# Kernel tuning notes

Hardware: AMD Instinct MI355X
Metric: run time of the kernel (lower is better)

## Reference

```python
import jax, jax.numpy as jnp
import numpy as np

N = 50000
E = 800000
IN_C = 128
HID_C = 64
OUT_C = 64
HEADS = 4
NEG_SLOPE = 0.2


def setup_inputs() -> dict:
    key = jax.random.key(0)
    ks = jax.random.split(key, 12)
    x = jax.random.normal(ks[0], (N, IN_C), dtype=jnp.float32)
    edge_index = jax.random.randint(ks[1], (2, E), 0, N, dtype=jnp.int32)
    s = 0.1
    # layer 1 params (GATConv: shared lin for src/dst, att vectors per head, bias over H*C)
    W1 = jax.random.normal(ks[2], (IN_C, HEADS * HID_C), dtype=jnp.float32) * s
    att_src1 = jax.random.normal(ks[3], (HEADS, HID_C), dtype=jnp.float32) * s
    att_dst1 = jax.random.normal(ks[4], (HEADS, HID_C), dtype=jnp.float32) * s
    b1 = jnp.zeros((HEADS * HID_C,), dtype=jnp.float32)
    # layer 2 params
    W2 = jax.random.normal(ks[5], (HEADS * HID_C, HEADS * OUT_C), dtype=jnp.float32) * s
    att_src2 = jax.random.normal(ks[6], (HEADS, OUT_C), dtype=jnp.float32) * s
    att_dst2 = jax.random.normal(ks[7], (HEADS, OUT_C), dtype=jnp.float32) * s
    b2 = jnp.zeros((HEADS * OUT_C,), dtype=jnp.float32)
    return {"x": x, "edge_index": edge_index,
            "W1": W1, "att_src1": att_src1, "att_dst1": att_dst1, "b1": b1,
            "W2": W2, "att_src2": att_src2, "att_dst2": att_dst2, "b2": b2}


def _segment_softmax(e, dst, n):
    # e: [E, H], softmax over edges sharing the same dst node, per head
    m = jax.ops.segment_max(e, dst, num_segments=n)        # [N, H]
    ex = jnp.exp(e - m[dst])
    z = jax.ops.segment_sum(ex, dst, num_segments=n)       # [N, H]
    return ex / (z[dst] + 1e-16)


def _gat_layer(x, src, dst, W, att_src, att_dst, bias, heads, out_c):
    n = x.shape[0]
    h = (x @ W).reshape(n, heads, out_c)                   # [N, H, C]
    a_s = jnp.einsum('nhc,hc->nh', h, att_src)             # [N, H]
    a_d = jnp.einsum('nhc,hc->nh', h, att_dst)
    e = jax.nn.leaky_relu(a_s[src] + a_d[dst], NEG_SLOPE)  # [E, H]
    alpha = _segment_softmax(e, dst, n)                    # [E, H]
    msg = alpha[:, :, None] * h[src]                       # [E, H, C]
    out = jax.ops.segment_sum(msg, dst, num_segments=n)    # [N, H, C]
    return out.reshape(n, heads * out_c) + bias


def reference(x, edge_index, W1, att_src1, att_dst1, b1, W2, att_src2, att_dst2, b2):
    # PyG GATConv adds self-loops by default
    loops = jnp.arange(N, dtype=edge_index.dtype)
    src = jnp.concatenate([edge_index[0], loops])
    dst = jnp.concatenate([edge_index[1], loops])
    h = jax.nn.elu(_gat_layer(x, src, dst, W1, att_src1, att_dst1, b1, HEADS, HID_C))
    out = jax.nn.elu(_gat_layer(h, src, dst, W2, att_src2, att_dst2, b2, HEADS, OUT_C))
    return out  # [N, HEADS*OUT_C]
```

## Files before the change

kernel.cpp:

```cpp
#include <hip/hip_runtime.h>
#include <hip/hip_fp16.h>
#include <math.h>


#define LEAKY_SLOPE 0.2f

typedef __attribute__((ext_vector_type(8))) short short8v;
typedef __attribute__((ext_vector_type(8))) _Float16 half8v;
typedef __attribute__((ext_vector_type(4))) float float4v;


__global__ void prep_kernel(const float* __restrict__ W1, __half* __restrict__ Bt1,
                            const float* __restrict__ W2, __half* __restrict__ Bt2,
                            const float* __restrict__ x, __half* __restrict__ x_h,
                            const int* __restrict__ ei, int* __restrict__ cnt,
                            int E, int N, int xblocks) {
    int b = blockIdx.x;
    if (b < 128) {
        int idx = b * 256 + threadIdx.x;
        int k = idx >> 8, c = idx & 255;
        Bt1[c * 128 + k] = __float2half(W1[idx]);
    } else if (b < 384) {
        int idx = (b - 128) * 256 + threadIdx.x;
        int k = idx >> 8, c = idx & 255;
        Bt2[c * 256 + k] = __float2half(W2[idx]);
    } else if (b < 384 + xblocks) {
        int t = (b - 384) * 256 + threadIdx.x;
        if (t < N * 32) {
            float4 v = *(const float4*)&x[(size_t)t * 4];
            __half2 h01 = __floats2half2_rn(v.x, v.y);
            __half2 h23 = __floats2half2_rn(v.z, v.w);
            uint2 pk = {*(unsigned*)&h01, *(unsigned*)&h23};
            *(uint2*)&x_h[(size_t)t * 4] = pk;
        }
    } else {
        int e = (b - 384 - xblocks) * 256 + threadIdx.x;
        if (e < E + N) {
            int dst = (e < E) ? ei[E + e] : (e - E);
            atomicAdd(&cnt[dst], 1);
        }
    }
}


__global__ __launch_bounds__(1024) void scan_block(const int* __restrict__ cnt,
                                                   int* __restrict__ row_start,
                                                   int* __restrict__ partials,
                                                   int n) {
    __shared__ int wsum[16];
    int tid = threadIdx.x, lane = tid & 63, wid = tid >> 6;
    int gi = blockIdx.x * 1024 + tid;
    int v = (gi < n) ? ((cnt[gi] + 1) & ~1) : 0;
    int x = v;
#pragma unroll
    for (int off = 1; off < 64; off <<= 1) {
        int y = __shfl_up(x, off, 64);
        if (lane >= off) x += y;
    }
    if (lane == 63) wsum[wid] = x;
    __syncthreads();
    if (wid == 0 && lane < 16) {
        int w = wsum[lane];
#pragma unroll
        for (int off = 1; off < 16; off <<= 1) {
            int y = __shfl_up(w, off, 16);
            if (lane >= off) w += y;
        }
        wsum[lane] = w;
    }
    __syncthreads();
    int excl = x - v + ((wid > 0) ? wsum[wid - 1] : 0);
    if (gi < n) row_start[gi] = excl;
    if (tid == 1023) partials[blockIdx.x] = wsum[15];
}

__global__ __launch_bounds__(1024) void scan_add(int* __restrict__ row_start,
                                                 const int* __restrict__ partials,
                                                 int n, int nb) {
    __shared__ int spart[2];
    if (threadIdx.x < 64) {
        int lane = threadIdx.x;
        int v = (lane < nb) ? partials[lane] : 0;
        int x = v;
#pragma unroll
        for (int off = 1; off < 64; off <<= 1) {
            int y = __shfl_up(x, off, 64);
            if (lane >= off) x += y;
        }
        if (lane == (int)blockIdx.x) spart[0] = x - v;
        if (lane == nb - 1) spart[1] = x;
    }
    __syncthreads();
    int gi = blockIdx.x * 1024 + threadIdx.x;
    if (gi < n) row_start[gi] += spart[0];
    if (gi == 0) row_start[n] = spart[1];
}

__global__ void scatter_kernel(const int* __restrict__ ei,
                               const int* __restrict__ row_start,
                               int* __restrict__ fill,
                               int2* __restrict__ edge_sd, int E, int Etot) {
    int e = blockIdx.x * blockDim.x + threadIdx.x;
    if (e >= Etot) return;
    int src, dst;
    if (e < E) { src = ei[e]; dst = ei[E + e]; }
    else       { src = e - E; dst = e - E; }
    int pos = row_start[dst] + atomicAdd(&fill[dst], 1);
    edge_sd[pos] = make_int2(src, dst);
}

__device__ __forceinline__ uint4 make_rec(int src, int dst,
                                          const __half* __restrict__ a_s_h,
                                          const float* __restrict__ a_d) {
    if (src < 0) {
        uint4 z = {0u, 0u, 0u, 0u};
        return z;
    }
    uint2 as2 = *(const uint2*)&a_s_h[(size_t)src * 4];
    float4 ad4 = *(const float4*)&a_d[(size_t)dst * 4];
    float2 f01 = __half22float2(*(const __half2*)&as2.x);
    float2 f23 = __half22float2(*(const __half2*)&as2.y);
    float e0 = f01.x + ad4.x, e1 = f01.y + ad4.y;
    float e2 = f23.x + ad4.z, e3 = f23.y + ad4.w;
    e0 = (e0 > 0.f) ? e0 : LEAKY_SLOPE * e0;
    e1 = (e1 > 0.f) ? e1 : LEAKY_SLOPE * e1;
    e2 = (e2 > 0.f) ? e2 : LEAKY_SLOPE * e2;
    e3 = (e3 > 0.f) ? e3 : LEAKY_SLOPE * e3;
    __half2 w01 = __floats2half2_rn(__expf(e0), __expf(e1));
    __half2 w23 = __floats2half2_rn(__expf(e2), __expf(e3));
    uint4 r = {(unsigned)src, *(unsigned*)&w01, *(unsigned*)&w23, 0u};
    return r;
}

__global__ void fill_rec(const int4* __restrict__ edge_sd2,
                         const __half* __restrict__ a_s_h,
                         const float* __restrict__ a_d,
                         uint4* __restrict__ rec, int npairs) {
    int i = blockIdx.x * blockDim.x + threadIdx.x;
    if (i >= npairs) return;
    int4 sd = edge_sd2[i];
    uint4 r0 = make_rec(sd.x, sd.y, a_s_h, a_d);
    uint4 r1 = make_rec(sd.z, sd.w, a_s_h, a_d);
    rec[2 * i] = r0;
    rec[2 * i + 1] = r1;
}


template <int K>
__global__ __launch_bounds__(256) void gemm_mfma(
    const __half* __restrict__ Ah, const __half* __restrict__ Bt,
    __half* __restrict__ Ch,
    const float* __restrict__ att_src, const float* __restrict__ att_dst,
    __half* __restrict__ a_s_out, float* __restrict__ a_d_out, int M) {
    __shared__ short As[128][40];
    __shared__ short Bs[128][40];

    const int col0 = (blockIdx.x & 1) * 128;
    const int row0 = (blockIdx.x >> 1) * 128;
    const int tid = threadIdx.x;
    const int lane = tid & 63;
    const int wave = tid >> 6;
    const int wr = wave >> 1, wc = wave & 1;
    const int quad = lane >> 4, lc = lane & 15;

    float4v acc[4][4] = {};

    const short* Abits = (const short*)Ah;
    const short* Bbits = (const short*)Bt;

    const int sr = tid >> 2;
    const int ko = (tid & 3) * 8;
    const int ga0 = row0 + sr, ga1 = ga0 + 64;
    const size_t gb0 = (size_t)(col0 + sr) * K + ko;
    const size_t gb1 = (size_t)(col0 + sr + 64) * K + ko;

    short8v pa0, pa1, pb0, pb1;
#define LOADT(k0)                                                          \
    {                                                                      \
        pa0 = {}; pa1 = {};                                                \
        if (ga0 < M) pa0 = *(const short8v*)&Abits[(size_t)ga0 * K + (k0) + ko]; \
        if (ga1 < M) pa1 = *(const short8v*)&Abits[(size_t)ga1 * K + (k0) + ko]; \
        pb0 = *(const short8v*)&Bbits[gb0 + (k0)];                         \
        pb1 = *(const short8v*)&Bbits[gb1 + (k0)];                         \
    }

    LOADT(0);

#pragma unroll
    for (int k0 = 0; k0 < K; k0 += 32) {
        *(short8v*)&As[sr][ko] = pa0;
        *(short8v*)&As[sr + 64][ko] = pa1;
        *(short8v*)&Bs[sr][ko] = pb0;
        *(short8v*)&Bs[sr + 64][ko] = pb1;
        __syncthreads();

        if (k0 + 32 < K) LOADT(k0 + 32);

        half8v a[4], bv[4];
#pragma unroll
        for (int mt = 0; mt < 4; mt++) {
            int r = wr * 64 + mt * 16 + lc;
            a[mt] = *(const half8v*)&As[r][quad * 8];
        }
#pragma unroll
        for (int nt = 0; nt < 4; nt++) {
            int n = wc * 64 + nt * 16 + lc;
            bv[nt] = *(const half8v*)&Bs[n][quad * 8];
        }
#pragma unroll
        for (int mt = 0; mt < 4; mt++)
#pragma unroll
            for (int nt = 0; nt < 4; nt++)
                acc[mt][nt] = __builtin_amdgcn_mfma_f32_16x16x32_f16(
                    a[mt], bv[nt], acc[mt][nt], 0, 0, 0);
        __syncthreads();
    }
#undef LOADT

    const int head = (col0 >> 6) + wc;
    float as_c[4], ad_c[4];
#pragma unroll
    for (int nt = 0; nt < 4; nt++) {
        as_c[nt] = att_src[head * 64 + nt * 16 + lc];
        ad_c[nt] = att_dst[head * 64 + nt * 16 + lc];
    }

#pragma unroll
    for (int mt = 0; mt < 4; mt++) {
#pragma unroll
        for (int r = 0; r < 4; r++) {
            int gr = row0 + wr * 64 + mt * 16 + quad * 4 + r;
            float ps = 0.f, pd = 0.f;
#pragma unroll
            for (int nt = 0; nt < 4; nt++) {
                float c = acc[mt][nt][r];
                ps = fmaf(c, as_c[nt], ps);
                pd = fmaf(c, ad_c[nt], pd);
                if (gr < M)
                    Ch[(size_t)gr * 256 + col0 + wc * 64 + nt * 16 + lc] =
                        __float2half(c);
            }
#pragma unroll
            for (int off = 1; off < 16; off <<= 1) {
                ps += __shfl_xor(ps, off, 64);
                pd += __shfl_xor(pd, off, 64);
            }
            if (lc == 0 && gr < M) {
                a_s_out[gr * 4 + head] = __float2half(ps);
                a_d_out[gr * 4 + head] = pd;
            }
        }
    }
}


template <bool OUT_HALF>
__global__ __launch_bounds__(256) void gat_aggregate(
    const __half* __restrict__ hh, const uint4* __restrict__ rec,
    const int* __restrict__ row_start, const float* __restrict__ bias,
    void* __restrict__ outp, int n) {
    int node = (blockIdx.x * blockDim.x + threadIdx.x) >> 6;
    if (node >= n) return;
    int lane = threadIdx.x & 63;
    int half = lane >> 5, l32 = lane & 31;
    int head = l32 >> 3;
    unsigned wsh = (head & 1) << 4;

    int beg = row_start[node];
    int end = row_start[node + 1];

    float l = 0.f;
    float acc[8] = {};

    uint4 r0 = rec[beg + half];
    uint4 r1 = rec[beg + 2 + half];
    uint4 r2 = rec[beg + 4 + half];
    uint4 r3 = rec[beg + 6 + half];

#define GATH(rr) (*(const uint4*)&hh[(size_t)(rr).x * 256 + l32 * 8])
#define PROC(rr, vv)                                                      \
    {                                                                     \
        unsigned u = (head & 2) ? (rr).z : (rr).y;                        \
        unsigned short us = (unsigned short)(u >> wsh);                   \
        float w = __half2float(*(const __half*)&us);                      \
        l += w;                                                           \
        const __half2* hp = (const __half2*)&(vv);                        \
        float2 f0 = __half22float2(hp[0]);                                \
        float2 f1 = __half22float2(hp[1]);                                \
        float2 f2 = __half22float2(hp[2]);                                \
        float2 f3 = __half22float2(hp[3]);                                \
        acc[0] = fmaf(w, f0.x, acc[0]); acc[1] = fmaf(w, f0.y, acc[1]);   \
        acc[2] = fmaf(w, f1.x, acc[2]); acc[3] = fmaf(w, f1.y, acc[3]);   \
        acc[4] = fmaf(w, f2.x, acc[4]); acc[5] = fmaf(w, f2.y, acc[5]);   \
        acc[6] = fmaf(w, f3.x, acc[6]); acc[7] = fmaf(w, f3.y, acc[7]);   \
    }

    uint4 h0 = GATH(r0);
    uint4 h1 = GATH(r1);
    uint4 h2 = GATH(r2);
    uint4 h3;

    int p = beg;
    while (p < end) {
        h3 = GATH(r3);
        PROC(r0, h0);
        r0 = rec[p + 8 + half];
        p += 2;
        if (p >= end) break;
        h0 = GATH(r0);
        PROC(r1, h1);
        r1 = rec[p + 8 + half];
        p += 2;
        if (p >= end) break;
        h1 = GATH(r1);
        PROC(r2, h2);
        r2 = rec[p + 8 + half];
        p += 2;
        if (p >= end) break;
        h2 = GATH(r2);
        PROC(r3, h3);
        r3 = rec[p + 8 + half];
        p += 2;
    }
#undef GATH
#undef PROC

    l += __shfl_xor(l, 32);
#pragma unroll
    for (int j = 0; j < 8; j++) acc[j] += __shfl_xor(acc[j], 32);

    if (half == 0) {
        float rcp = 1.f / l;
        float4 b0 = *(const float4*)&bias[l32 * 8];
        float4 b1 = *(const float4*)&bias[l32 * 8 + 4];
        float o[8];
        o[0] = fmaf(acc[0], rcp, b0.x); o[1] = fmaf(acc[1], rcp, b0.y);
        o[2] = fmaf(acc[2], rcp, b0.z); o[3] = fmaf(acc[3], rcp, b0.w);
        o[4] = fmaf(acc[4], rcp, b1.x); o[5] = fmaf(acc[5], rcp, b1.y);
        o[6] = fmaf(acc[6], rcp, b1.z); o[7] = fmaf(acc[7], rcp, b1.w);
#pragma unroll
        for (int j = 0; j < 8; j++)
            o[j] = (o[j] > 0.f) ? o[j] : __expf(o[j]) - 1.f;
        if constexpr (OUT_HALF) {
            __half2 q0 = __floats2half2_rn(o[0], o[1]);
            __half2 q1 = __floats2half2_rn(o[2], o[3]);
            __half2 q2 = __floats2half2_rn(o[4], o[5]);
            __half2 q3 = __floats2half2_rn(o[6], o[7]);
            uint4 pk = {*(unsigned*)&q0, *(unsigned*)&q1,
                        *(unsigned*)&q2, *(unsigned*)&q3};
            __half* outh = (__half*)outp;
            *(uint4*)&outh[(size_t)node * 256 + l32 * 8] = pk;
        } else {
            float* outf = (float*)outp;
            *(float4*)&outf[(size_t)node * 256 + l32 * 8] = *(float4*)&o[0];
            *(float4*)&outf[(size_t)node * 256 + l32 * 8 + 4] = *(float4*)&o[4];
        }
    }
}


extern "C" void kernel_launch(void* const* d_in, const int* in_sizes, int n_in,
                              void* d_out, int out_size, void* d_ws, size_t ws_size,
                              hipStream_t stream) {
    const float* x   = (const float*)d_in[0];
    const int*   ei  = (const int*)d_in[1];
    const float* W1  = (const float*)d_in[2];
    const float* as1 = (const float*)d_in[3];
    const float* ad1 = (const float*)d_in[4];
    const float* b1  = (const float*)d_in[5];
    const float* W2  = (const float*)d_in[6];
    const float* as2 = (const float*)d_in[7];
    const float* ad2 = (const float*)d_in[8];
    const float* b2  = (const float*)d_in[9];
    float* out = (float*)d_out;

    const int N = in_sizes[0] / 128;
    const int E = in_sizes[1] / 2;
    const int Etot = E + N;
    const int EtotMax = (Etot + N + 9) & ~1;
    const int NB = (N + 1023) / 1024;

    __half* h_half = (__half*)d_ws;
    __half* x1_h   = h_half + (size_t)N * 256;
    uint4*  rec    = (uint4*)(x1_h + (size_t)N * 256);
    __half* a_s_h  = (__half*)(rec + EtotMax);
    float*  a_d    = (float*)(a_s_h + (size_t)N * 4);
    __half* Bt1    = (__half*)(a_d + (size_t)N * 4);
    __half* Bt2    = Bt1 + 256 * 128;
    int*    cnt    = (int*)(Bt2 + 256 * 256);
    int*    fill   = cnt + N;
    int*    row_st = fill + N;
    int2*   edge_sd = (int2*)(row_st + (N + 2));
    int*    partials = (int*)(edge_sd + EtotMax);

    hipMemsetAsync(cnt, 0, sizeof(int) * 2 * (size_t)N, stream);
    hipMemsetAsync(edge_sd, 0xFF, sizeof(int2) * (size_t)EtotMax, stream);

    const int xblocks = (N * 32 + 255) / 256;
    const int eblocks = (Etot + 255) / 256;
    prep_kernel<<<384 + xblocks + eblocks, 256, 0, stream>>>(
        W1, Bt1, W2, Bt2, x, x1_h, ei, cnt, E, N, xblocks);

    scan_block<<<NB, 1024, 0, stream>>>(cnt, row_st, partials, N);
    scan_add<<<NB, 1024, 0, stream>>>(row_st, partials, N, NB);
    scatter_kernel<<<eblocks, 256, 0, stream>>>(ei, row_st, fill, edge_sd, E, Etot);

    dim3 ggrid(2 * ((N + 127) / 128));
    int ablocks = (N + 3) / 4;
    int npairs = EtotMax / 2;
    int fblocks = (npairs + 255) / 256;

    gemm_mfma<128><<<ggrid, 256, 0, stream>>>(x1_h, Bt1, h_half,
                                              as1, ad1, a_s_h, a_d, N);
    fill_rec<<<fblocks, 256, 0, stream>>>((const int4*)edge_sd, a_s_h, a_d,
                                          rec, npairs);
    gat_aggregate<true><<<ablocks, 256, 0, stream>>>(h_half, rec, row_st,
                                                     b1, x1_h, N);
    gemm_mfma<256><<<ggrid, 256, 0, stream>>>(x1_h, Bt2, h_half,
                                              as2, ad2, a_s_h, a_d, N);
    fill_rec<<<fblocks, 256, 0, stream>>>((const int4*)edge_sd, a_s_h, a_d,
                                          rec, npairs);
    gat_aggregate<false><<<ablocks, 256, 0, stream>>>(h_half, rec, row_st,
                                                      b2, out, N);
}
```

Before: 380.6 us.

## Fuse edge scatter into first GEMM launch and sentinel fill into prep kernel

Removes the standalone scatter kernel by appending extra blocks to the layer-1 GEMM grid that perform the CSR scatter concurrently with the matrix multiply. The scan_add kernel now initializes the fill counters with row starts, so scatter needs only one atomic and no row_start read. The sentinel memset of edge_sd is folded into prep_kernel as extra blocks, and the remaining memset shrinks to just cnt. This saves kernel launches and memset dispatches and overlaps scatter with GEMM, at the cost of mixing heterogeneous blocks in one grid.

```diff
diff --git a/kernel.cpp b/kernel.cpp
--- a/kernel.cpp
+++ b/kernel.cpp
@@ -14,7 +14,8 @@
                             const float* __restrict__ W2, __half* __restrict__ Bt2,
                             const float* __restrict__ x, __half* __restrict__ x_h,
                             const int* __restrict__ ei, int* __restrict__ cnt,
-                            int E, int N, int xblocks) {
+                            uint4* __restrict__ edge_sd_v, int nsent,
+                            int E, int N, int xblocks, int eblocks) {
     int b = blockIdx.x;
     if (b < 128) {
         int idx = b * 256 + threadIdx.x;
@@ -33,11 +34,17 @@
             uint2 pk = {*(unsigned*)&h01, *(unsigned*)&h23};
             *(uint2*)&x_h[(size_t)t * 4] = pk;
         }
-    } else {
+    } else if (b < 384 + xblocks + eblocks) {
         int e = (b - 384 - xblocks) * 256 + threadIdx.x;
         if (e < E + N) {
             int dst = (e < E) ? ei[E + e] : (e - E);
             atomicAdd(&cnt[dst], 1);
+        }
+    } else {
+        int t = (b - 384 - xblocks - eblocks) * 256 + threadIdx.x;
+        if (t < nsent) {
+            uint4 s = {0xFFFFFFFFu, 0xFFFFFFFFu, 0xFFFFFFFFu, 0xFFFFFFFFu};
+            edge_sd_v[t] = s;
         }
     }
 }
@@ -76,6 +83,7 @@
 
 __global__ __launch_bounds__(1024) void scan_add(int* __restrict__ row_start,
                                                  const int* __restrict__ partials,
+                                                 int* __restrict__ fill,
                                                  int n, int nb) {
     __shared__ int spart[2];
     if (threadIdx.x < 64) {
@@ -92,21 +100,12 @@
     }
     __syncthreads();
     int gi = blockIdx.x * 1024 + threadIdx.x;
-    if (gi < n) row_start[gi] += spart[0];
+    if (gi < n) {
+        int v = row_start[gi] + spart[0];
+        row_start[gi] = v;
+        fill[gi] = v;
+    }
     if (gi == 0) row_start[n] = spart[1];
-}
-
-__global__ void scatter_kernel(const int* __restrict__ ei,
-                               const int* __restrict__ row_start,
-                               int* __restrict__ fill,
-                               int2* __restrict__ edge_sd, int E, int Etot) {
-    int e = blockIdx.x * blockDim.x + threadIdx.x;
-    if (e >= Etot) return;
-    int src, dst;
-    if (e < E) { src = ei[e]; dst = ei[E + e]; }
-    else       { src = e - E; dst = e - E; }
-    int pos = row_start[dst] + atomicAdd(&fill[dst], 1);
-    edge_sd[pos] = make_int2(src, dst);
 }
 
 __device__ __forceinline__ uint4 make_rec(int src, int dst,
@@ -146,14 +145,30 @@
 }
 
 
-template <int K>
+template <int K, bool SCAT>
 __global__ __launch_bounds__(256) void gemm_mfma(
     const __half* __restrict__ Ah, const __half* __restrict__ Bt,
     __half* __restrict__ Ch,
     const float* __restrict__ att_src, const float* __restrict__ att_dst,
-    __half* __restrict__ a_s_out, float* __restrict__ a_d_out, int M) {
+    __half* __restrict__ a_s_out, float* __restrict__ a_d_out, int M,
+    const int* __restrict__ ei, int* __restrict__ fill,
+    int2* __restrict__ edge_sd, int E, int Etot, int ngemm) {
     __shared__ short As[128][40];
     __shared__ short Bs[128][40];
+
+    if constexpr (SCAT) {
+        if ((int)blockIdx.x >= ngemm) {
+            int e = ((int)blockIdx.x - ngemm) * 256 + threadIdx.x;
+            if (e < Etot) {
+                int src, dst;
+                if (e < E) { src = ei[e]; dst = ei[E + e]; }
+                else       { src = e - E; dst = e - E; }
+                int pos = atomicAdd(&fill[dst], 1);
+                edge_sd[pos] = make_int2(src, dst);
+            }
+            return;
+        }
+    }
 
     const int col0 = (blockIdx.x & 1) * 128;
     const int row0 = (blockIdx.x >> 1) * 128;
@@ -393,31 +408,34 @@
     int2*   edge_sd = (int2*)(row_st + (N + 2));
     int*    partials = (int*)(edge_sd + EtotMax);
 
-    hipMemsetAsync(cnt, 0, sizeof(int) * 2 * (size_t)N, stream);
-    hipMemsetAsync(edge_sd, 0xFF, sizeof(int2) * (size_t)EtotMax, stream);
+    hipMemsetAsync(cnt, 0, sizeof(int) * (size_t)N, stream);
 
     const int xblocks = (N * 32 + 255) / 256;
     const int eblocks = (Etot + 255) / 256;
-    prep_kernel<<<384 + xblocks + eblocks, 256, 0, stream>>>(
-        W1, Bt1, W2, Bt2, x, x1_h, ei, cnt, E, N, xblocks);
+    const int nsent = EtotMax / 2;
+    const int sblocks = (nsent + 255) / 256;
+    prep_kernel<<<384 + xblocks + eblocks + sblocks, 256, 0, stream>>>(
+        W1, Bt1, W2, Bt2, x, x1_h, ei, cnt, (uint4*)edge_sd, nsent,
+        E, N, xblocks, eblocks);
 
     scan_block<<<NB, 1024, 0, stream>>>(cnt, row_st, partials, N);
-    scan_add<<<NB, 1024, 0, stream>>>(row_st, partials, N, NB);
-    scatter_kernel<<<eblocks, 256, 0, stream>>>(ei, row_st, fill, edge_sd, E, Etot);
-
-    dim3 ggrid(2 * ((N + 127) / 128));
+    scan_add<<<NB, 1024, 0, stream>>>(row_st, partials, fill, N, NB);
+
+    const int ngemm = 2 * ((N + 127) / 128);
     int ablocks = (N + 3) / 4;
     int npairs = EtotMax / 2;
     int fblocks = (npairs + 255) / 256;
 
-    gemm_mfma<128><<<ggrid, 256, 0, stream>>>(x1_h, Bt1, h_half,
-                                              as1, ad1, a_s_h, a_d, N);
+    gemm_mfma<128, true><<<ngemm + eblocks, 256, 0, stream>>>(
+        x1_h, Bt1, h_half, as1, ad1, a_s_h, a_d, N,
+        ei, fill, edge_sd, E, Etot, ngemm);
     fill_rec<<<fblocks, 256, 0, stream>>>((const int4*)edge_sd, a_s_h, a_d,
                                           rec, npairs);
     gat_aggregate<true><<<ablocks, 256, 0, stream>>>(h_half, rec, row_st,
                                                      b1, x1_h, N);
-    gemm_mfma<256><<<ggrid, 256, 0, stream>>>(x1_h, Bt2, h_half,
-                                              as2, ad2, a_s_h, a_d, N);
+    gemm_mfma<256, false><<<ngemm, 256, 0, stream>>>(
+        x1_h, Bt2, h_half, as2, ad2, a_s_h, a_d, N,
+        nullptr, nullptr, nullptr, 0, 0, ngemm);
     fill_rec<<<fblocks, 256, 0, stream>>>((const int4*)edge_sd, a_s_h, a_d,
                                           rec, npairs);
     gat_aggregate<false><<<ablocks, 256, 0, stream>>>(h_half, rec, row_st,
```

After: 391.3 us. 1.03x slower.
